# Performance work log

Hardware: AMD Instinct MI355X
Metric: run time of the kernel (lower is better)

The kernel has to match this reference:

```python
import jax, jax.numpy as jnp
import numpy as np
import math

N = 8192
DIM = 256

def setup_inputs() -> dict:
    key = jax.random.key(0)
    k1, k2, k3 = jax.random.split(key, 3)
    h = jax.random.normal(k1, (N, DIM), dtype=jnp.float32)
    # xavier_uniform with gain=1.414 for square [dim, dim] matrices
    gain = 1.414
    bound = gain * math.sqrt(6.0 / (DIM + DIM))
    Wq = jax.random.uniform(k2, (DIM, DIM), dtype=jnp.float32, minval=-bound, maxval=bound)
    Wk = jax.random.uniform(k3, (DIM, DIM), dtype=jnp.float32, minval=-bound, maxval=bound)
    return {"h": h, "Wq": Wq, "Wk": Wk}

def reference(h, Wq, Wk):
    dim = h.shape[1]
    q = h @ Wq                                   # [N, dim]
    k = h @ Wk                                   # [N, dim]
    e = (q @ k.T) / jnp.sqrt(jnp.asarray(dim, h.dtype))  # [N, N]
    attention = jax.nn.softmax(e, axis=1)        # row-wise softmax
    attention = attention.mean(axis=0)           # [N], column-mean over rows
    x = attention @ h                            # [dim]
    return x
```

## Files before the change

kernel.cpp:

```cpp
#include <hip/hip_runtime.h>
#include <cstdint>
#include <cstddef>


#define N_ROWS 8192
#define DIM    256

typedef __bf16 bf16x8 __attribute__((ext_vector_type(8)));
typedef unsigned short u16x8 __attribute__((ext_vector_type(8)));
typedef float f32x16 __attribute__((ext_vector_type(16)));
typedef float f32x4  __attribute__((ext_vector_type(4)));

__device__ __forceinline__ uint16_t f2bf(float f) {
    uint32_t u = __float_as_uint(f);
    uint32_t r = (u + 0x7fffu + ((u >> 16) & 1u)) >> 16;
    return (uint16_t)r;
}

__device__ __forceinline__ void gld16(const void* gsrc, void* ldst) {
    __builtin_amdgcn_global_load_lds(
        (const __attribute__((address_space(1))) unsigned int*)gsrc,
        (__attribute__((address_space(3))) unsigned int*)ldst, 16, 0, 0);
}

__device__ __forceinline__ size_t frag_off(int i, int d) {
    int tile = i >> 5, il = i & 31;
    int a0 = d >> 4, hi = (d >> 3) & 1, j = d & 7;
    return (size_t)tile * 8192 + (size_t)((a0 * 64) + il + 32 * hi) * 8 + j;
}

__global__ __launch_bounds__(256) void proj_kernel(
        const float* __restrict__ h, const float* __restrict__ Wq,
        const float* __restrict__ Wk, uint16_t* __restrict__ qf,
        uint16_t* __restrict__ kf, float* __restrict__ l_arr,
        float* __restrict__ c_arr, float* __restrict__ out) {
    __shared__ alignas(16) uint16_t wlds[8 * 8 * 64 * 8];
    const int tid = threadIdx.x;
    const int lane = tid & 63, wave = tid >> 6;
    const int which = blockIdx.x & 1;
    const int rb = blockIdx.x >> 1;

    if (blockIdx.x < 32)       l_arr[blockIdx.x * 256 + tid] = 0.0f;
    else if (blockIdx.x < 64)  c_arr[(blockIdx.x - 32) * 256 + tid] = 0.0f;
    else if (blockIdx.x == 64) out[tid] = 0.0f;

    const float* __restrict__ W = which ? Wk : Wq;
    uint16_t* __restrict__ dst = which ? kf : qf;
    const float scale = which ? 1.0f : 0.0625f;
    const int rowbase = rb * 64 + wave * 16;

    bf16x8 afrag[8];
    {
        const int r = rowbase + (lane & 15);
        const float* hp = h + (size_t)r * DIM + ((lane >> 4) * 8);
#pragma unroll
        for (int a0 = 0; a0 < 8; a0++) {
            float4 f0 = *(const float4*)(hp + a0 * 32);
            float4 f1 = *(const float4*)(hp + a0 * 32 + 4);
            u16x8 f;
            f[0] = f2bf(f0.x); f[1] = f2bf(f0.y); f[2] = f2bf(f0.z); f[3] = f2bf(f0.w);
            f[4] = f2bf(f1.x); f[5] = f2bf(f1.y); f[6] = f2bf(f1.z); f[7] = f2bf(f1.w);
            afrag[a0] = __builtin_bit_cast(bf16x8, f);
        }
    }

    for (int p = 0; p < 2; p++) {
        __syncthreads();
        for (int s = tid; s < 4096; s += 256) {
            int ctl = s >> 9, a0 = (s >> 6) & 7, l = s & 63;
            int n = (p * 8 + ctl) * 16 + (l & 15);
            int kb = a0 * 32 + (l >> 4) * 8;
            u16x8 f;
#pragma unroll
            for (int j = 0; j < 8; j++) f[j] = f2bf(W[(size_t)(kb + j) * DIM + n]);
            *(u16x8*)&wlds[(size_t)s * 8] = f;
        }
        __syncthreads();
#pragma unroll
        for (int ctl = 0; ctl < 8; ctl++) {
            const int ct = p * 8 + ctl;
            f32x4 acc;
#pragma unroll
            for (int i = 0; i < 4; i++) acc[i] = 0.0f;
#pragma unroll
            for (int a0 = 0; a0 < 8; a0++) {
                bf16x8 bfrag = __builtin_bit_cast(bf16x8,
                    *(const u16x8*)&wlds[(size_t)((ctl * 8 + a0) * 64 + lane) * 8]);
                acc = __builtin_amdgcn_mfma_f32_16x16x32_bf16(afrag[a0], bfrag, acc, 0, 0, 0);
            }
            const int dcol = ct * 16 + (lane & 15);
            const int rbas = rowbase + ((lane >> 4) << 2);
#pragma unroll
            for (int reg = 0; reg < 4; reg++) {
                dst[frag_off(rbas + reg, dcol)] = f2bf(acc[reg] * scale);
            }
        }
    }
}

template <int MODE>
__global__ __launch_bounds__(256, 4) void pass_kernel(
        const uint16_t* __restrict__ qf, const uint16_t* __restrict__ kf,
        float* __restrict__ l_arr, float* __restrict__ c_arr) {
    __shared__ alignas(16) uint16_t ktile[2][8192];
    __shared__ float c_lds[512];
    const int tid = threadIdx.x, lane = tid & 63, wave = tid >> 6;
    const int rb = blockIdx.x >> 4, cc = blockIdx.x & 15;
    const int t0 = rb * 4 + wave;

    bf16x8 qreg[16];
    {
        const uint4* qp = (const uint4*)qf;
#pragma unroll
        for (int a0 = 0; a0 < 16; a0++)
            qreg[a0] = __builtin_bit_cast(bf16x8, qp[(size_t)t0 * 1024 + a0 * 64 + lane]);
    }

    float rs[16];
    float rr[16];
    if (MODE == 0) {
#pragma unroll
        for (int reg = 0; reg < 16; reg++) rs[reg] = 0.0f;
    } else {
#pragma unroll
        for (int reg = 0; reg < 16; reg++) {
            int row = rb * 128 + wave * 32 + (reg & 3) + 8 * (reg >> 2) + 4 * (lane >> 5);
            rr[reg] = 1.0f / (8192.0f * l_arr[row]);
        }
        for (int i = tid; i < 512; i += 256) c_lds[i] = 0.0f;
    }

    const char* ksrc = (const char*)(kf + (size_t)cc * 16 * 8192);

    {
        const char* s0 = ksrc + wave * 4096 + lane * 16;
        char* d0 = (char*)&ktile[0][0] + wave * 4096;
#pragma unroll
        for (int it = 0; it < 4; it++) gld16(s0 + it * 1024, d0 + it * 1024);
    }

    for (int step = 0; step < 16; step++) {
        __syncthreads();
        if (step < 15) {
            const char* sn = ksrc + (step + 1) * 16384 + wave * 4096 + lane * 16;
            char* dn = (char*)&ktile[(step + 1) & 1][0] + wave * 4096;
#pragma unroll
            for (int it = 0; it < 4; it++) gld16(sn + it * 1024, dn + it * 1024);
        }

        const uint16_t* kt = &ktile[step & 1][0];
        f32x16 acc;
#pragma unroll
        for (int i = 0; i < 16; i++) acc[i] = 0.0f;
#pragma unroll
        for (int a0 = 0; a0 < 16; a0++) {
            bf16x8 bfrag = __builtin_bit_cast(bf16x8,
                *(const u16x8*)&kt[(size_t)(a0 * 64 + lane) * 8]);
            acc = __builtin_amdgcn_mfma_f32_32x32x16_bf16(qreg[a0], bfrag, acc, 0, 0, 0);
        }

        if (MODE == 0) {
#pragma unroll
            for (int reg = 0; reg < 16; reg++) rs[reg] += __expf(acc[reg]);
        } else {
            float s = 0.0f;
#pragma unroll
            for (int reg = 0; reg < 16; reg++) s += __expf(acc[reg]) * rr[reg];
            s += __shfl_xor(s, 32);
            if (lane < 32) atomicAdd(&c_lds[step * 32 + lane], s);
        }
    }

    if (MODE == 0) {
#pragma unroll
        for (int reg = 0; reg < 16; reg++) {
            float v = rs[reg];
            v += __shfl_xor(v, 1);  v += __shfl_xor(v, 2);  v += __shfl_xor(v, 4);
            v += __shfl_xor(v, 8);  v += __shfl_xor(v, 16);
            if ((lane & 31) == 0) {
                int row = rb * 128 + wave * 32 + (reg & 3) + 8 * (reg >> 2) + 4 * (lane >> 5);
                atomicAdd(&l_arr[row], v);
            }
        }
    } else {
        __syncthreads();
        for (int i = tid; i < 512; i += 256) atomicAdd(&c_arr[cc * 512 + i], c_lds[i]);
    }
}

__global__ __launch_bounds__(256) void finish_kernel(
        const float* __restrict__ h, const float* __restrict__ c_arr,
        float* __restrict__ out) {
    const int d = threadIdx.x;
    const int j0 = blockIdx.x * 32;
    float acc = 0.0f;
    for (int j = j0; j < j0 + 32; j++) acc += c_arr[j] * h[(size_t)j * DIM + d];
    atomicAdd(&out[d], acc);
}

extern "C" void kernel_launch(void* const* d_in, const int* in_sizes, int n_in,
                              void* d_out, int out_size, void* d_ws, size_t ws_size,
                              hipStream_t stream) {
    const float* h  = (const float*)d_in[0];
    const float* Wq = (const float*)d_in[1];
    const float* Wk = (const float*)d_in[2];

    uint16_t* qf = (uint16_t*)d_ws;
    uint16_t* kf = qf + (size_t)N_ROWS * DIM;
    float* l_arr = (float*)((char*)d_ws + (size_t)8 * 1024 * 1024);
    float* c_arr = l_arr + N_ROWS;
    float* out = (float*)d_out;

    proj_kernel<<<256, 256, 0, stream>>>(h, Wq, Wk, qf, kf, l_arr, c_arr, out);
    pass_kernel<0><<<1024, 256, 0, stream>>>(qf, kf, l_arr, c_arr);
    pass_kernel<1><<<1024, 256, 0, stream>>>(qf, kf, l_arr, c_arr);
    finish_kernel<<<256, 256, 0, stream>>>(h, c_arr, out);
}
```

Measured before the change: 165.6 us.

## Split MFMA accumulators, defer exp, restructure projection to 32x32 MFMA

The attention pass kernels now accumulate QK^T into two independent MFMA chains (even/odd k-slices) and evaluate the exp of the previous step's tile while the current tile's MFMAs issue. This shortens dependent MFMA chains and overlaps transcendental work with matrix work. The projection kernel is rewritten to load W coalesced as float4 into a 64KB LDS buffer and use 32x32x16 MFMA over 32-row tiles with twice as many blocks. Launch bounds drop to 3 waves/SIMD, and the finish kernel uses fewer, longer blocks. Extra accumulator registers and lower occupancy are the tradeoff.

```diff
diff --git a/kernel.cpp b/kernel.cpp
--- a/kernel.cpp
+++ b/kernel.cpp
@@ -9,7 +9,6 @@
 typedef __bf16 bf16x8 __attribute__((ext_vector_type(8)));
 typedef unsigned short u16x8 __attribute__((ext_vector_type(8)));
 typedef float f32x16 __attribute__((ext_vector_type(16)));
-typedef float f32x4  __attribute__((ext_vector_type(4)));
 
 __device__ __forceinline__ uint16_t f2bf(float f) {
     uint32_t u = __float_as_uint(f);
@@ -34,11 +33,10 @@
         const float* __restrict__ Wk, uint16_t* __restrict__ qf,
         uint16_t* __restrict__ kf, float* __restrict__ l_arr,
         float* __restrict__ c_arr, float* __restrict__ out) {
-    __shared__ alignas(16) uint16_t wlds[8 * 8 * 64 * 8];
-    const int tid = threadIdx.x;
-    const int lane = tid & 63, wave = tid >> 6;
+    __shared__ alignas(16) uint16_t wb[256 * 128];
+    const int tid = threadIdx.x, lane = tid & 63, wave = tid >> 6;
     const int which = blockIdx.x & 1;
-    const int rb = blockIdx.x >> 1;
+    const int rt = blockIdx.x >> 1;
 
     if (blockIdx.x < 32)       l_arr[blockIdx.x * 256 + tid] = 0.0f;
     else if (blockIdx.x < 64)  c_arr[(blockIdx.x - 32) * 256 + tid] = 0.0f;
@@ -47,16 +45,15 @@
     const float* __restrict__ W = which ? Wk : Wq;
     uint16_t* __restrict__ dst = which ? kf : qf;
     const float scale = which ? 1.0f : 0.0625f;
-    const int rowbase = rb * 64 + wave * 16;
-
-    bf16x8 afrag[8];
+
+    bf16x8 afrag[16];
     {
-        const int r = rowbase + (lane & 15);
-        const float* hp = h + (size_t)r * DIM + ((lane >> 4) * 8);
-#pragma unroll
-        for (int a0 = 0; a0 < 8; a0++) {
-            float4 f0 = *(const float4*)(hp + a0 * 32);
-            float4 f1 = *(const float4*)(hp + a0 * 32 + 4);
+        const int r = rt * 32 + (lane & 31);
+        const float* hp = h + (size_t)r * DIM + ((lane >> 5) * 8);
+#pragma unroll
+        for (int a0 = 0; a0 < 16; a0++) {
+            float4 f0 = *(const float4*)(hp + a0 * 16);
+            float4 f1 = *(const float4*)(hp + a0 * 16 + 4);
             u16x8 f;
             f[0] = f2bf(f0.x); f[1] = f2bf(f0.y); f[2] = f2bf(f0.z); f[3] = f2bf(f0.w);
             f[4] = f2bf(f1.x); f[5] = f2bf(f1.y); f[6] = f2bf(f1.z); f[7] = f2bf(f1.w);
@@ -66,46 +63,51 @@
 
     for (int p = 0; p < 2; p++) {
         __syncthreads();
-        for (int s = tid; s < 4096; s += 256) {
-            int ctl = s >> 9, a0 = (s >> 6) & 7, l = s & 63;
-            int n = (p * 8 + ctl) * 16 + (l & 15);
-            int kb = a0 * 32 + (l >> 4) * 8;
+#pragma unroll
+        for (int c = 0; c < 32; c++) {
+            int f = c * 256 + tid;
+            int k = f >> 5, nc = (f & 31) * 4;
+            float4 w4 = *(const float4*)&W[(size_t)k * DIM + p * 128 + nc];
+            ushort4 b;
+            b.x = f2bf(w4.x); b.y = f2bf(w4.y); b.z = f2bf(w4.z); b.w = f2bf(w4.w);
+            *(ushort4*)&wb[k * 128 + nc] = b;
+        }
+        __syncthreads();
+
+        const int ct = wave;
+        f32x16 acc;
+#pragma unroll
+        for (int i = 0; i < 16; i++) acc[i] = 0.0f;
+        const int cl = ct * 32 + (lane & 31);
+#pragma unroll
+        for (int a0 = 0; a0 < 16; a0++) {
+            const int kb = a0 * 16 + (lane >> 5) * 8;
             u16x8 f;
 #pragma unroll
-            for (int j = 0; j < 8; j++) f[j] = f2bf(W[(size_t)(kb + j) * DIM + n]);
-            *(u16x8*)&wlds[(size_t)s * 8] = f;
-        }
-        __syncthreads();
-#pragma unroll
-        for (int ctl = 0; ctl < 8; ctl++) {
-            const int ct = p * 8 + ctl;
-            f32x4 acc;
-#pragma unroll
-            for (int i = 0; i < 4; i++) acc[i] = 0.0f;
-#pragma unroll
-            for (int a0 = 0; a0 < 8; a0++) {
-                bf16x8 bfrag = __builtin_bit_cast(bf16x8,
-                    *(const u16x8*)&wlds[(size_t)((ctl * 8 + a0) * 64 + lane) * 8]);
-                acc = __builtin_amdgcn_mfma_f32_16x16x32_bf16(afrag[a0], bfrag, acc, 0, 0, 0);
-            }
-            const int dcol = ct * 16 + (lane & 15);
-            const int rbas = rowbase + ((lane >> 4) << 2);
-#pragma unroll
-            for (int reg = 0; reg < 4; reg++) {
-                dst[frag_off(rbas + reg, dcol)] = f2bf(acc[reg] * scale);
-            }
+            for (int j = 0; j < 8; j++) f[j] = wb[(kb + j) * 128 + cl];
+            acc = __builtin_amdgcn_mfma_f32_32x32x16_bf16(
+                afrag[a0], __builtin_bit_cast(bf16x8, f), acc, 0, 0, 0);
+        }
+        const int dcol = p * 128 + ct * 32 + (lane & 31);
+        const int rb0 = rt * 32 + 4 * (lane >> 5);
+#pragma unroll
+        for (int reg = 0; reg < 16; reg++) {
+            int row = rb0 + (reg & 3) + 8 * (reg >> 2);
+            dst[frag_off(row, dcol)] = f2bf(acc[reg] * scale);
         }
     }
 }
 
 template <int MODE>
-__global__ __launch_bounds__(256, 4) void pass_kernel(
+__global__ __launch_bounds__(256, 3) void pass_kernel(
         const uint16_t* __restrict__ qf, const uint16_t* __restrict__ kf,
         float* __restrict__ l_arr, float* __restrict__ c_arr) {
     __shared__ alignas(16) uint16_t ktile[2][8192];
     __shared__ float c_lds[512];
     const int tid = threadIdx.x, lane = tid & 63, wave = tid >> 6;
-    const int rb = blockIdx.x >> 4, cc = blockIdx.x & 15;
+    const int bid = blockIdx.x;
+    const int cc = (bid & 7) | (((bid >> 3) & 1) << 3);
+    const int rb = bid >> 4;
     const int t0 = rb * 4 + wave;
 
     bf16x8 qreg[16];
@@ -139,6 +141,10 @@
         for (int it = 0; it < 4; it++) gld16(s0 + it * 1024, d0 + it * 1024);
     }
 
+    f32x16 ae, ao;
+#pragma unroll
+    for (int i = 0; i < 16; i++) { ae[i] = 0.0f; ao[i] = 0.0f; }
+
     for (int step = 0; step < 16; step++) {
         __syncthreads();
         if (step < 15) {
@@ -148,30 +154,36 @@
             for (int it = 0; it < 4; it++) gld16(sn + it * 1024, dn + it * 1024);
         }
 
+        if (step > 0) {
+            if (MODE == 0) {
+#pragma unroll
+                for (int reg = 0; reg < 16; reg++) rs[reg] += __expf(ae[reg] + ao[reg]);
+            } else {
+                float s = 0.0f;
+#pragma unroll
+                for (int reg = 0; reg < 16; reg++) s += __expf(ae[reg] + ao[reg]) * rr[reg];
+                s += __shfl_xor(s, 32);
+                if (lane < 32) atomicAdd(&c_lds[(step - 1) * 32 + lane], s);
+            }
+#pragma unroll
+            for (int i = 0; i < 16; i++) { ae[i] = 0.0f; ao[i] = 0.0f; }
+        }
+
         const uint16_t* kt = &ktile[step & 1][0];
-        f32x16 acc;
-#pragma unroll
-        for (int i = 0; i < 16; i++) acc[i] = 0.0f;
-#pragma unroll
-        for (int a0 = 0; a0 < 16; a0++) {
-            bf16x8 bfrag = __builtin_bit_cast(bf16x8,
-                *(const u16x8*)&kt[(size_t)(a0 * 64 + lane) * 8]);
-            acc = __builtin_amdgcn_mfma_f32_32x32x16_bf16(qreg[a0], bfrag, acc, 0, 0, 0);
-        }
-
-        if (MODE == 0) {
-#pragma unroll
-            for (int reg = 0; reg < 16; reg++) rs[reg] += __expf(acc[reg]);
-        } else {
-            float s = 0.0f;
-#pragma unroll
-            for (int reg = 0; reg < 16; reg++) s += __expf(acc[reg]) * rr[reg];
-            s += __shfl_xor(s, 32);
-            if (lane < 32) atomicAdd(&c_lds[step * 32 + lane], s);
+#pragma unroll
+        for (int a0 = 0; a0 < 8; a0++) {
+            bf16x8 b0 = __builtin_bit_cast(bf16x8,
+                *(const u16x8*)&kt[(size_t)((2 * a0) * 64 + lane) * 8]);
+            bf16x8 b1 = __builtin_bit_cast(bf16x8,
+                *(const u16x8*)&kt[(size_t)((2 * a0 + 1) * 64 + lane) * 8]);
+            ae = __builtin_amdgcn_mfma_f32_32x32x16_bf16(qreg[2 * a0], b0, ae, 0, 0, 0);
+            ao = __builtin_amdgcn_mfma_f32_32x32x16_bf16(qreg[2 * a0 + 1], b1, ao, 0, 0, 0);
         }
     }
 
     if (MODE == 0) {
+#pragma unroll
+        for (int reg = 0; reg < 16; reg++) rs[reg] += __expf(ae[reg] + ao[reg]);
 #pragma unroll
         for (int reg = 0; reg < 16; reg++) {
             float v = rs[reg];
@@ -183,6 +195,11 @@
             }
         }
     } else {
+        float s = 0.0f;
+#pragma unroll
+        for (int reg = 0; reg < 16; reg++) s += __expf(ae[reg] + ao[reg]) * rr[reg];
+        s += __shfl_xor(s, 32);
+        if (lane < 32) atomicAdd(&c_lds[15 * 32 + lane], s);
         __syncthreads();
         for (int i = tid; i < 512; i += 256) atomicAdd(&c_arr[cc * 512 + i], c_lds[i]);
     }
@@ -192,9 +209,9 @@
         const float* __restrict__ h, const float* __restrict__ c_arr,
         float* __restrict__ out) {
     const int d = threadIdx.x;
-    const int j0 = blockIdx.x * 32;
+    const int j0 = blockIdx.x * 64;
     float acc = 0.0f;
-    for (int j = j0; j < j0 + 32; j++) acc += c_arr[j] * h[(size_t)j * DIM + d];
+    for (int j = j0; j < j0 + 64; j++) acc += c_arr[j] * h[(size_t)j * DIM + d];
     atomicAdd(&out[d], acc);
 }
 
@@ -211,8 +228,8 @@
     float* c_arr = l_arr + N_ROWS;
     float* out = (float*)d_out;
 
-    proj_kernel<<<256, 256, 0, stream>>>(h, Wq, Wk, qf, kf, l_arr, c_arr, out);
+    proj_kernel<<<512, 256, 0, stream>>>(h, Wq, Wk, qf, kf, l_arr, c_arr, out);
     pass_kernel<0><<<1024, 256, 0, stream>>>(qf, kf, l_arr, c_arr);
     pass_kernel<1><<<1024, 256, 0, stream>>>(qf, kf, l_arr, c_arr);
-    finish_kernel<<<256, 256, 0, stream>>>(h, c_arr, out);
-}
+    finish_kernel<<<128, 256, 0, stream>>>(h, c_arr, out);
+}
```

After: 180.3 us. +8.8%, slower.
